# Kernel tuning notes

Hardware: AMD Instinct MI355X
Metric: run time of the kernel (lower is better)

Reference implementation:

```python
import jax, jax.numpy as jnp
import numpy as np

B, S, D, H = 2, 2048, 1024, 16
E = D // H  # per-head dim_q = dim_k = 64
LN_EPS = 1e-5


def setup_inputs() -> dict:
    key = jax.random.key(0)
    ks = jax.random.split(key, 12)
    s_in = 1.0 / np.sqrt(D)
    s_cat = 1.0 / np.sqrt(H * E)
    return {
        "q": jax.random.normal(ks[0], (B, S, D), jnp.float32),
        "k": jax.random.normal(ks[1], (B, S, D), jnp.float32),
        "v": jax.random.normal(ks[2], (B, S, D), jnp.float32),
        # stacked per-head projection weights [H, D, E] (acts as x @ W + b per head)
        "Wq": jax.random.uniform(ks[3], (H, D, E), jnp.float32, -s_in, s_in),
        "bq": jax.random.uniform(ks[4], (H, E), jnp.float32, -s_in, s_in),
        "Wk": jax.random.uniform(ks[5], (H, D, E), jnp.float32, -s_in, s_in),
        "bk": jax.random.uniform(ks[6], (H, E), jnp.float32, -s_in, s_in),
        "Wv": jax.random.uniform(ks[7], (H, D, E), jnp.float32, -s_in, s_in),
        "bv": jax.random.uniform(ks[8], (H, E), jnp.float32, -s_in, s_in),
        # output linear: [H*E, D]
        "Wo": jax.random.uniform(ks[9], (H * E, D), jnp.float32, -s_cat, s_cat),
        "bo": jax.random.uniform(ks[10], (D,), jnp.float32, -s_cat, s_cat),
        # LayerNorm affine params
        "gamma": jnp.ones((D,), jnp.float32),
        "beta": jnp.zeros((D,), jnp.float32),
    }


def _attention(q, k, v, Wq, bq, Wk, bk, Wv, bv, Wo, bo, gamma, beta):
    # per-head projections: [B,H,S,E]
    qh = jnp.einsum('bsd,hde->bhse', q, Wq) + bq[None, :, None, :]
    kh = jnp.einsum('bsd,hde->bhse', k, Wk) + bk[None, :, None, :]
    vh = jnp.einsum('bsd,hde->bhse', v, Wv) + bv[None, :, None, :]
    scale = jnp.asarray(E, qh.dtype) ** 0.5
    scores = jnp.einsum('bhse,bhte->bhst', qh, kh) / scale  # [B,H,S,S]
    attn = jax.nn.softmax(scores, axis=-1)
    ctx = jnp.einsum('bhst,bhte->bhse', attn, vh)  # [B,H,S,E]
    # concat heads -> [B,S,H*E], then output linear
    cat = ctx.transpose(0, 2, 1, 3).reshape(q.shape[0], q.shape[1], H * E)
    out = cat @ Wo + bo  # [B,S,D]
    # Residual (dropout = identity in eval) + LayerNorm
    x = q + out
    mu = jnp.mean(x, axis=-1, keepdims=True)
    var = jnp.mean((x - mu) ** 2, axis=-1, keepdims=True)
    return (x - mu) * jax.lax.rsqrt(var + LN_EPS) * gamma + beta


def reference(q, k, v, Wq, bq, Wk, bk, Wv, bv, Wo, bo, gamma, beta):
    return _attention(q, k, v, Wq, bq, Wk, bk, Wv, bv, Wo, bo, gamma, beta)
```

## Files before the change

### kernel.cpp

```cpp
#include <hip/hip_runtime.h>
#include <stdint.h>

#define B_  2
#define S_  2048
#define D_  1024
#define H_  16
#define E_  64
#define BH_ 32
#define M_  4096
#define NSPLIT 4
#define KCHUNK (S_ / NSPLIT)

typedef __bf16 bf16x8 __attribute__((ext_vector_type(8)));
typedef float  f32x4  __attribute__((ext_vector_type(4)));
typedef float  f32x16 __attribute__((ext_vector_type(16)));
typedef unsigned short u16;

#define QSCALE 0.180336880f

#define EXP2(x) __builtin_amdgcn_exp2f(x)

__device__ __forceinline__ u16 f2bf(float f) {
  uint32_t u = __builtin_bit_cast(uint32_t, f);
  u = (u + 0x7FFFu + ((u >> 16) & 1u)) >> 16;
  return (u16)u;
}

__device__ __forceinline__ uint32_t pkbf(float lo, float hi) {
  __bf16 a = (__bf16)lo, b = (__bf16)hi;
  return (uint32_t)__builtin_bit_cast(u16, a) |
         ((uint32_t)__builtin_bit_cast(u16, b) << 16);
}

__device__ __forceinline__ bf16x8 load_frag(const u16* p) {
  uint4 v = *(const uint4*)p;
  return __builtin_bit_cast(bf16x8, v);
}

__device__ __forceinline__ float bf2f(u16 u) {
  return __builtin_bit_cast(float, (uint32_t)u << 16);
}

__device__ __forceinline__ void gload16(const void* g, void* l) {
  auto gp = reinterpret_cast<const uint32_t __attribute__((address_space(1)))*>(
      reinterpret_cast<uintptr_t>(g));
  auto lp = reinterpret_cast<uint32_t __attribute__((address_space(3)))*>(
      reinterpret_cast<uintptr_t>(l));
  __builtin_amdgcn_global_load_lds(gp, lp, 16, 0, 0);
}

__global__ __launch_bounds__(256) void transpose_cvt3w(
    const float* __restrict__ Wq, const float* __restrict__ Wk,
    const float* __restrict__ Wv, u16* __restrict__ out)
{
  __shared__ float tile[32][33];
  const int z = blockIdx.z, sel = z >> 4, b = z & 15;
  const float* in = (sel == 0 ? Wq : (sel == 1 ? Wk : Wv)) + (size_t)b * 65536;
  u16* o = out + (size_t)sel * 1048576 + (size_t)b * 65536;
  const int R = 1024, C = 64;
  const int c0 = blockIdx.x * 32, r0 = blockIdx.y * 32;
  const int tx = threadIdx.x, ty = threadIdx.y;
#pragma unroll
  for (int j = 0; j < 32; j += 8)
    tile[ty + j][tx] = in[(size_t)(r0 + ty + j) * C + c0 + tx];
  __syncthreads();
#pragma unroll
  for (int j = 0; j < 32; j += 8)
    o[(size_t)(c0 + ty + j) * R + r0 + tx] = f2bf(tile[tx][ty + j]);
}

__global__ __launch_bounds__(256) void transpose_cvt(
    const float* __restrict__ in, u16* __restrict__ out, int R, int C)
{
  __shared__ float tile[32][33];
  const int c0 = blockIdx.x * 32, r0 = blockIdx.y * 32;
  const int tx = threadIdx.x, ty = threadIdx.y;
#pragma unroll
  for (int j = 0; j < 32; j += 8)
    tile[ty + j][tx] = in[(size_t)(r0 + ty + j) * C + c0 + tx];
  __syncthreads();
#pragma unroll
  for (int j = 0; j < 32; j += 8)
    out[(size_t)(c0 + ty + j) * R + r0 + tx] = f2bf(tile[tx][ty + j]);
}

__global__ __launch_bounds__(256) void cvt3_bf16(
    const float* __restrict__ a, const float* __restrict__ b,
    const float* __restrict__ c, u16* __restrict__ out, int n)
{
  const float* src = blockIdx.y == 0 ? a : (blockIdx.y == 1 ? b : c);
  u16* dst = out + (size_t)blockIdx.y * n;
  int i = (blockIdx.x * 256 + threadIdx.x) * 4;
  if (i < n) {
    float4 v = *(const float4*)(src + i);
    ushort4 o;
    o.x = f2bf(v.x); o.y = f2bf(v.y); o.z = f2bf(v.z); o.w = f2bf(v.w);
    *(ushort4*)(dst + i) = o;
  }
}

template<int MODE>
__global__ __launch_bounds__(256) void gemm128(
    const u16* __restrict__ A, const u16* __restrict__ Bt,
    const float* __restrict__ b0, const float* __restrict__ b1,
    const float* __restrict__ b2, const float* __restrict__ resid,
    u16* __restrict__ outQ, u16* __restrict__ outK, u16* __restrict__ outV,
    float* __restrict__ outX)
{
  __shared__ __align__(16) u16 As[2][128 * 64];
  __shared__ __align__(16) u16 Bs[2][128 * 64];
  const int K  = D_;
  const int id = blockIdx.x;
  const int xcd = id & 7, slot = id >> 3;
  int mi_, ni_;
  if (MODE == 0) { ni_ = slot % 24; mi_ = (xcd << 2) | (slot / 24); }
  else           { ni_ = slot & 7;  mi_ = (xcd << 2) | (slot >> 3); }
  const int m0 = mi_ * 128;
  const int n0 = ni_ * 128;
  const int tid = threadIdx.x;
  const int w = tid >> 6, l = tid & 63;
  const int wr = w >> 1, wc = w & 1;
  const int ql = l & 31, h2 = l >> 5;

  const u16* Ause = A;
  const u16* Buse = Bt;
  const float* bias = b0;
  int third = 0, nloc = n0;
  if (MODE == 0) {
    third = n0 >> 10;
    nloc  = n0 & 1023;
    Ause  = A  + (size_t)third * M_ * D_;
    Buse  = Bt + (size_t)third * D_ * D_;
    bias  = third == 0 ? b0 : (third == 1 ? b1 : b2);
  }

  const int rr = l >> 3, gce = ((l & 7) ^ (l >> 3)) * 8;
  const u16* aptr[4];
  const u16* bptr[4];
#pragma unroll
  for (int c = 0; c < 4; ++c) {
    const int chunk = w * 4 + c;
    aptr[c] = Ause + (size_t)(m0 + chunk * 8 + rr) * K + gce;
    bptr[c] = Buse + (size_t)(nloc + chunk * 8 + rr) * K + gce;
  }

  const int swz = ql & 7;
  f32x16 acc[2][2] = {};

#pragma unroll
  for (int c = 0; c < 4; ++c) {
    const int chunk = w * 4 + c;
    gload16(aptr[c], &As[0][chunk * 8 * 64]);
    gload16(bptr[c], &Bs[0][chunk * 8 * 64]);
  }

  int cur = 0;
  for (int k0 = 0; k0 < K; k0 += 64) {
    __syncthreads();
    const int nxt = k0 + 64;
    if (nxt < K) {
#pragma unroll
      for (int c = 0; c < 4; ++c) {
        const int chunk = w * 4 + c;
        gload16(aptr[c] + nxt, &As[cur ^ 1][chunk * 8 * 64]);
        gload16(bptr[c] + nxt, &Bs[cur ^ 1][chunk * 8 * 64]);
      }
    }
#pragma unroll
    for (int ks = 0; ks < 4; ++ks) {
      const int ch = ((ks * 2 + h2) ^ swz) * 8;
      bf16x8 af[2], bf[2];
#pragma unroll
      for (int mi = 0; mi < 2; ++mi)
        af[mi] = load_frag(&As[cur][(wr * 64 + mi * 32 + ql) * 64 + ch]);
#pragma unroll
      for (int ni = 0; ni < 2; ++ni)
        bf[ni] = load_frag(&Bs[cur][(wc * 64 + ni * 32 + ql) * 64 + ch]);
#pragma unroll
      for (int mi = 0; mi < 2; ++mi)
#pragma unroll
        for (int ni = 0; ni < 2; ++ni)
          acc[mi][ni] = __builtin_amdgcn_mfma_f32_32x32x16_bf16(
              af[mi], bf[ni], acc[mi][ni], 0, 0, 0);
    }
    cur ^= 1;
  }

  const int rbase = m0 + wr * 64;
  const int cbase = nloc + wc * 64;
#pragma unroll
  for (int mi = 0; mi < 2; ++mi) {
#pragma unroll
    for (int ni = 0; ni < 2; ++ni) {
      const int col = cbase + ni * 32 + ql;
      const float bv = bias[col];
      if (MODE == 0) {
        const int h = col >> 6, e = col & 63;
        if (third < 2) {
          u16* dst = third == 0 ? outQ : outK;
          const float sc = third == 0 ? QSCALE : 1.f;
#pragma unroll
          for (int r = 0; r < 16; ++r) {
            int row = rbase + mi * 32 + (r & 3) + 8 * (r >> 2) + 4 * h2;
            int bb = row >> 11, s = row & (S_ - 1);
            dst[((size_t)(bb * H_ + h) * S_ + s) * E_ + e] =
                f2bf((acc[mi][ni][r] + bv) * sc);
          }
        } else {
#pragma unroll
          for (int g = 0; g < 4; ++g) {
            int s0 = rbase + mi * 32 + ((g >> 1) << 4) + (h2 << 3) + ((g & 1) << 2);
            int bb = s0 >> 11, srel = s0 & (S_ - 1);
            ushort4 o;
            o.x = f2bf(acc[mi][ni][4 * g + 0] + bv);
            o.y = f2bf(acc[mi][ni][4 * g + 1] + bv);
            o.z = f2bf(acc[mi][ni][4 * g + 2] + bv);
            o.w = f2bf(acc[mi][ni][4 * g + 3] + bv);
            *(ushort4*)(&outV[((size_t)(bb * H_ + h) * E_ + e) * S_ + srel]) = o;
          }
        }
      } else {
#pragma unroll
        for (int r = 0; r < 16; ++r) {
          int row = rbase + mi * 32 + (r & 3) + 8 * (r >> 2) + 4 * h2;
          size_t idx = (size_t)row * D_ + col;
          outX[idx] = acc[mi][ni][r] + bv + resid[idx];
        }
      }
    }
  }
}

__global__ __launch_bounds__(256, 4) void attn_kernel(
    const u16* __restrict__ qh, const u16* __restrict__ kh,
    const u16* __restrict__ vT, u16* __restrict__ pA, u16* __restrict__ pB,
    float* __restrict__ ml)
{
  __shared__ __align__(16) u16 Ks[2][64 * 64];
  __shared__ __align__(16) u16 Vs[2][64 * 64];
  const int o = blockIdx.x;
  const int xcd = o & 7, slot = o >> 3;
  const int bh    = (xcd << 2) | (slot >> 6);
  const int rem   = slot & 63;
  const int split = rem >> 4;
  const int q0    = (rem & 15) * 128;
  const int kst = split * KCHUNK;
  const int tid = threadIdx.x;
  const int w = tid >> 6, l = tid & 63;
  const int ql = l & 31;
  const int h  = l >> 5;
  const int qg = q0 + w * 32 + ql;

  const size_t PSZ = (size_t)BH_ * S_ * E_;
  u16* po = split < 2 ? pA + (size_t)split * PSZ : pB + (size_t)(split - 2) * PSZ;

  const u16* qrow = qh + ((size_t)bh * S_ + qg) * E_;
  bf16x8 bq_[4];
#pragma unroll
  for (int es = 0; es < 4; ++es)
    bq_[es] = load_frag(qrow + es * 16 + h * 8);

  f32x16 oacc[2] = {};
  float lloc = 0.f;

  const int srow = w * 8 + (l >> 3);
  const int gch  = (l & 7) ^ (l >> 3);
  const u16* kbase = kh + (size_t)bh * S_ * E_;
  const u16* vbase = vT + (size_t)bh * E_ * S_;
  const int swz = (ql & 7);

  auto stage = [&](int buf, int t0) {
#pragma unroll
    for (int p = 0; p < 2; ++p) {
      gload16(kbase + (size_t)(t0 + p * 32 + srow) * E_ + gch * 8,
              &Ks[buf][p * 2048 + w * 512]);
      gload16(vbase + (size_t)(p * 32 + srow) * S_ + t0 + gch * 8,
              &Vs[buf][p * 2048 + w * 512]);
    }
  };

  stage(0, kst);
  int cur = 0;
  for (int t0 = kst; t0 < kst + KCHUNK; t0 += 64) {
    __syncthreads();
    if (t0 + 64 < kst + KCHUNK) stage(cur ^ 1, t0 + 64);

#pragma unroll
    for (int kt = 0; kt < 2; ++kt) {
      f32x16 sacc = {};
#pragma unroll
      for (int es = 0; es < 4; ++es) {
        bf16x8 ak = load_frag(
            &Ks[cur][(kt * 32 + ql) * 64 + (((es * 2 + h) ^ swz) * 8)]);
        sacc = __builtin_amdgcn_mfma_f32_32x32x16_bf16(ak, bq_[es], sacc, 0, 0, 0);
      }

      float ps0 = 0.f, ps1 = 0.f, ps2 = 0.f, ps3 = 0.f;
#pragma unroll
      for (int i = 0; i < 16; i += 4) {
        float p0 = EXP2(sacc[i + 0]); sacc[i + 0] = p0; ps0 += p0;
        float p1 = EXP2(sacc[i + 1]); sacc[i + 1] = p1; ps1 += p1;
        float p2 = EXP2(sacc[i + 2]); sacc[i + 2] = p2; ps2 += p2;
        float p3 = EXP2(sacc[i + 3]); sacc[i + 3] = p3; ps3 += p3;
      }
      lloc += (ps0 + ps1) + (ps2 + ps3);

#pragma unroll
      for (int c2 = 0; c2 < 2; ++c2) {
        uint4 pw;
        pw.x = pkbf(sacc[8 * c2 + 0], sacc[8 * c2 + 1]);
        pw.y = pkbf(sacc[8 * c2 + 2], sacc[8 * c2 + 3]);
        pw.z = pkbf(sacc[8 * c2 + 4], sacc[8 * c2 + 5]);
        pw.w = pkbf(sacc[8 * c2 + 6], sacc[8 * c2 + 7]);
        bf16x8 pb = __builtin_bit_cast(bf16x8, pw);
        const int vch = ((kt * 2 + c2) * 2 + h) ^ swz;
#pragma unroll
        for (int eb = 0; eb < 2; ++eb) {
          bf16x8 av = load_frag(&Vs[cur][(eb * 32 + ql) * 64 + vch * 8]);
          oacc[eb] = __builtin_amdgcn_mfma_f32_32x32x16_bf16(av, pb, oacc[eb], 0, 0, 0);
        }
      }
    }
    cur ^= 1;
  }

  float l_ = lloc + __shfl_xor(lloc, 32);
  const float inv = 1.f / l_;
  const size_t rowbase = ((size_t)bh * S_ + qg) * E_;
#pragma unroll
  for (int eb = 0; eb < 2; ++eb)
#pragma unroll
    for (int g = 0; g < 4; ++g) {
      ushort4 o2;
      o2.x = f2bf(oacc[eb][4 * g + 0] * inv);
      o2.y = f2bf(oacc[eb][4 * g + 1] * inv);
      o2.z = f2bf(oacc[eb][4 * g + 2] * inv);
      o2.w = f2bf(oacc[eb][4 * g + 3] * inv);
      *(ushort4*)(&po[rowbase + eb * 32 + g * 8 + h * 4]) = o2;
    }
  if (h == 0)
    ml[(size_t)(split * BH_ + bh) * S_ + qg] = l_;
}

__global__ __launch_bounds__(256) void combine_kernel(
    const u16* __restrict__ pA, const u16* __restrict__ pB,
    const float* __restrict__ ml, u16* __restrict__ cat)
{
  const int idx = blockIdx.x * 256 + threadIdx.x;
  const int e  = (idx & 15) * 4;
  const int s  = (idx >> 4) & (S_ - 1);
  const int bh = idx >> 15;
  const size_t row = (size_t)bh * S_ + s;
  const size_t PSZ = (size_t)BH_ * S_ * E_;

  float li[NSPLIT], W = 0.f;
#pragma unroll
  for (int i = 0; i < NSPLIT; ++i) {
    li[i] = ml[(size_t)(i * BH_ + bh) * S_ + s];
    W += li[i];
  }
  const float invW = 1.f / W;

  float acc0 = 0.f, acc1 = 0.f, acc2 = 0.f, acc3 = 0.f;
#pragma unroll
  for (int i = 0; i < NSPLIT; ++i) {
    const u16* p = i < 2 ? pA + (size_t)i * PSZ : pB + (size_t)(i - 2) * PSZ;
    ushort4 u = *(const ushort4*)(&p[row * E_ + e]);
    const float wi = li[i] * invW;
    acc0 += wi * bf2f(u.x);
    acc1 += wi * bf2f(u.y);
    acc2 += wi * bf2f(u.z);
    acc3 += wi * bf2f(u.w);
  }
  ushort4 o;
  o.x = f2bf(acc0); o.y = f2bf(acc1); o.z = f2bf(acc2); o.w = f2bf(acc3);
  *(ushort4*)(&cat[((size_t)(bh >> 4) * S_ + s) * D_ + (bh & 15) * E_ + e]) = o;
}

__global__ __launch_bounds__(256) void layernorm_kernel(
    float* __restrict__ x, const float* __restrict__ gamma,
    const float* __restrict__ beta)
{
  __shared__ float red[8];
  const int row = blockIdx.x;
  float* p = x + (size_t)row * D_;
  const int tid = threadIdx.x;
  float4 v = *(const float4*)(p + tid * 4);
  float s  = v.x + v.y + v.z + v.w;
  float sq = v.x * v.x + v.y * v.y + v.z * v.z + v.w * v.w;
#pragma unroll
  for (int d = 1; d < 64; d <<= 1) {
    s  += __shfl_xor(s, d);
    sq += __shfl_xor(sq, d);
  }
  const int w = tid >> 6, l = tid & 63;
  if (l == 0) { red[w] = s; red[4 + w] = sq; }
  __syncthreads();
  float S1 = red[0] + red[1] + red[2] + red[3];
  float S2 = red[4] + red[5] + red[6] + red[7];
  float mu  = S1 * (1.f / D_);
  float var = S2 * (1.f / D_) - mu * mu;
  float rinv = rsqrtf(var + 1e-5f);
  float4 g  = *(const float4*)(gamma + tid * 4);
  float4 bt = *(const float4*)(beta + tid * 4);
  float4 o;
  o.x = (v.x - mu) * rinv * g.x + bt.x;
  o.y = (v.y - mu) * rinv * g.y + bt.y;
  o.z = (v.z - mu) * rinv * g.z + bt.z;
  o.w = (v.w - mu) * rinv * g.w + bt.w;
  *(float4*)(p + tid * 4) = o;
}

extern "C" void kernel_launch(void* const* d_in, const int* in_sizes, int n_in,
                              void* d_out, int out_size, void* d_ws, size_t ws_size,
                              hipStream_t stream) {
  (void)in_sizes; (void)n_in; (void)out_size; (void)ws_size;
  const float* q     = (const float*)d_in[0];
  const float* k     = (const float*)d_in[1];
  const float* v     = (const float*)d_in[2];
  const float* Wq    = (const float*)d_in[3];
  const float* bq    = (const float*)d_in[4];
  const float* Wk    = (const float*)d_in[5];
  const float* bk    = (const float*)d_in[6];
  const float* Wv    = (const float*)d_in[7];
  const float* bv    = (const float*)d_in[8];
  const float* Wo    = (const float*)d_in[9];
  const float* bo    = (const float*)d_in[10];
  const float* gamma = (const float*)d_in[11];
  const float* beta  = (const float*)d_in[12];

  char* ws = (char*)d_ws;
  u16* qkv_bf = (u16*)ws;
  u16* Wt     = (u16*)(ws + 25165824);
  u16* WoT    = (u16*)(ws + 31457280);
  u16* qhb    = (u16*)(ws + 33554432);
  u16* khb    = (u16*)(ws + 41943040);
  u16* vTb    = (u16*)(ws + 50331648);
  u16* cat    = qkv_bf;
  u16*   pA  = (u16*)d_out;
  u16*   pB  = (u16*)(ws + 8388608);
  float* mlb = (float*)(ws + 25165824);
  float* x   = (float*)d_out;

  dim3 tb(32, 8);
  transpose_cvt3w<<<dim3(2, 32, 48), tb, 0, stream>>>(Wq, Wk, Wv, Wt);
  transpose_cvt<<<dim3(32, 32, 1), tb, 0, stream>>>(Wo, WoT, 1024, 1024);
  cvt3_bf16<<<dim3(4096, 3), 256, 0, stream>>>(q, k, v, qkv_bf, M_ * D_);

  gemm128<0><<<768, 256, 0, stream>>>(qkv_bf, Wt, bq, bk, bv, nullptr,
                                      qhb, khb, vTb, nullptr);
  attn_kernel<<<2048, 256, 0, stream>>>(qhb, khb, vTb, pA, pB, mlb);
  combine_kernel<<<4096, 256, 0, stream>>>(pA, pB, mlb, cat);
  gemm128<1><<<256, 256, 0, stream>>>(cat, WoT, bo, nullptr, nullptr, q,
                                      nullptr, nullptr, nullptr, x);
  layernorm_kernel<<<4096, 256, 0, stream>>>(x, gamma, beta);
}
```

Measured before the change: 151.8 us.

## Load K and V fragments directly from global memory in attention kernel

Drops the double-buffered LDS staging of K and V tiles, along with the per-iteration __syncthreads, and has each wave load its MFMA operand fragments straight from global memory (relying on L1/L2). This removes LDS traffic, barriers and shared-memory footprint, which may raise occupancy. In exchange, all four waves in a block now load the same K/V data redundantly from cache, and global-load latency is exposed without explicit prefetch.

```diff
diff --git a/kernel.cpp b/kernel.cpp
--- a/kernel.cpp
+++ b/kernel.cpp
@@ -236,8 +236,6 @@
     const u16* __restrict__ vT, u16* __restrict__ pA, u16* __restrict__ pB,
     float* __restrict__ ml)
 {
-  __shared__ __align__(16) u16 Ks[2][64 * 64];
-  __shared__ __align__(16) u16 Vs[2][64 * 64];
   const int o = blockIdx.x;
   const int xcd = o & 7, slot = o >> 3;
   const int bh    = (xcd << 2) | (slot >> 6);
@@ -263,35 +261,17 @@
   f32x16 oacc[2] = {};
   float lloc = 0.f;
 
-  const int srow = w * 8 + (l >> 3);
-  const int gch  = (l & 7) ^ (l >> 3);
-  const u16* kbase = kh + (size_t)bh * S_ * E_;
-  const u16* vbase = vT + (size_t)bh * E_ * S_;
-  const int swz = (ql & 7);
-
-  auto stage = [&](int buf, int t0) {
-#pragma unroll
-    for (int p = 0; p < 2; ++p) {
-      gload16(kbase + (size_t)(t0 + p * 32 + srow) * E_ + gch * 8,
-              &Ks[buf][p * 2048 + w * 512]);
-      gload16(vbase + (size_t)(p * 32 + srow) * S_ + t0 + gch * 8,
-              &Vs[buf][p * 2048 + w * 512]);
-    }
-  };
-
-  stage(0, kst);
-  int cur = 0;
+  const u16* kx = kh + ((size_t)bh * S_ + ql) * E_ + h * 8;
+  const u16* vx = vT + ((size_t)bh * E_ + ql) * S_ + h * 8;
+
   for (int t0 = kst; t0 < kst + KCHUNK; t0 += 64) {
-    __syncthreads();
-    if (t0 + 64 < kst + KCHUNK) stage(cur ^ 1, t0 + 64);
-
 #pragma unroll
     for (int kt = 0; kt < 2; ++kt) {
+      const u16* krow = kx + (size_t)(t0 + kt * 32) * E_;
       f32x16 sacc = {};
 #pragma unroll
       for (int es = 0; es < 4; ++es) {
-        bf16x8 ak = load_frag(
-            &Ks[cur][(kt * 32 + ql) * 64 + (((es * 2 + h) ^ swz) * 8)]);
+        bf16x8 ak = load_frag(krow + es * 16);
         sacc = __builtin_amdgcn_mfma_f32_32x32x16_bf16(ak, bq_[es], sacc, 0, 0, 0);
       }
 
@@ -313,15 +293,14 @@
         pw.z = pkbf(sacc[8 * c2 + 4], sacc[8 * c2 + 5]);
         pw.w = pkbf(sacc[8 * c2 + 6], sacc[8 * c2 + 7]);
         bf16x8 pb = __builtin_bit_cast(bf16x8, pw);
-        const int vch = ((kt * 2 + c2) * 2 + h) ^ swz;
+        const int kofs = t0 + (kt * 2 + c2) * 16;
 #pragma unroll
         for (int eb = 0; eb < 2; ++eb) {
-          bf16x8 av = load_frag(&Vs[cur][(eb * 32 + ql) * 64 + vch * 8]);
+          bf16x8 av = load_frag(vx + (size_t)(eb * 32) * S_ + kofs);
           oacc[eb] = __builtin_amdgcn_mfma_f32_32x32x16_bf16(av, pb, oacc[eb], 0, 0, 0);
         }
       }
     }
-    cur ^= 1;
   }
 
   float l_ = lloc + __shfl_xor(lloc, 32);
```

Result: slower. 231.9 us (+52.8%).
